# Kernel tuning notes

Measured on AMD Instinct MI355X. Metric: run time of the kernel, lower is better.

Reference implementation:

```python
import jax, jax.numpy as jnp
import numpy as np

N = 200_000      # num_nodes
D = 32           # embedding_dim
E = 6_400_000    # num edges (avg degree 32)
L = 3            # num_layers


def setup_inputs() -> dict:
    key = jax.random.key(0)
    k1, k2, k3, k4 = jax.random.split(key, 4)
    # xavier_uniform init: bound = sqrt(6 / (fan_in + fan_out))
    bound = float(np.sqrt(6.0 / (N + D)))
    embedding = jax.random.uniform(k1, (N, D), minval=-bound, maxval=bound, dtype=jnp.float32)
    row_idx = jax.random.randint(k2, (E,), 0, N, dtype=jnp.int32)
    col_idx = jax.random.randint(k3, (E,), 0, N, dtype=jnp.int32)
    # normalized adjacency values (roughly 1/degree scale, like sym-normalized LightGCN adj)
    vals = jax.random.uniform(k4, (E,), minval=0.0, maxval=2.0 / 32.0, dtype=jnp.float32)
    return {"embedding": embedding, "vals": vals, "row_idx": row_idx,
            "col_idx": col_idx, "num_layers": L}


def reference(embedding, vals, row_idx, col_idx, num_layers):
    # LightGCN propagation: e^{l+1} = A @ e^{l} (sparse COO SpMM via gather + scatter-add),
    # output = mean over layer outputs [e^0, e^1, ..., e^L].
    n = embedding.shape[0]
    e = embedding
    acc = embedding  # running sum of layer outputs (fused, avoids stacking)
    for _ in range(num_layers):
        msgs = vals[:, None] * e[col_idx]                      # [E, D] gather + scale
        e = jax.ops.segment_sum(msgs, row_idx, num_segments=n)  # [N, D] scatter-add
        acc = acc + e
    return acc / jnp.asarray(num_layers + 1, dtype=embedding.dtype)
```

## Files before the change

### kernel.cpp

```cpp
#include <hip/hip_runtime.h>
#include <hip/hip_bf16.h>

#define DIM 32
#define BSHIFT 8
#define BROWS 256
#define CAP 12288
#define CHUNK 8192
#define KMAX 1024


__global__ void lgcn_bhist(const int* __restrict__ row,
                           int* __restrict__ bcount, int E, int K) {
    __shared__ int h[KMAX];
    int t = threadIdx.x;
    for (int b = t; b < K; b += blockDim.x) h[b] = 0;
    __syncthreads();
    for (int i = blockIdx.x * blockDim.x + t; i < E; i += gridDim.x * blockDim.x)
        atomicAdd(&h[row[i] >> BSHIFT], 1);
    __syncthreads();
    for (int b = t; b < K; b += blockDim.x)
        if (h[b]) atomicAdd(&bcount[b], h[b]);
}

__global__ void lgcn_bscan(const int* __restrict__ bcount,
                           int* __restrict__ bbase, int* __restrict__ bcursor, int K) {
    __shared__ int s[1024];
    int t = threadIdx.x;
    int v = (t < K) ? bcount[t] : 0;
    s[t] = v;
    __syncthreads();
    for (int off = 1; off < 1024; off <<= 1) {
        int u = (t >= off) ? s[t - off] : 0;
        __syncthreads();
        s[t] += u;
        __syncthreads();
    }
    if (t < K) {
        int excl = s[t] - v;
        bbase[t] = excl;
        bcursor[t] = excl;
    }
    if (t == 0) bbase[K] = s[1023];
}

__launch_bounds__(1024)
__global__ void lgcn_bin(const int* __restrict__ row, const int* __restrict__ col,
                         const float* __restrict__ vals, int* __restrict__ bcursor,
                         int2* __restrict__ binned, int E, int K) {
    __shared__ int hh[KMAX];
    __shared__ int lb[KMAX + 1];
    __shared__ int cur[KMAX];
    __shared__ int2 sbuf[CHUNK];
    int t = threadIdx.x;
    int base = blockIdx.x * CHUNK;
    int cnt = E - base;
    if (cnt > CHUNK) cnt = CHUNK;

    for (int b = t; b < K; b += 1024) hh[b] = 0;
    __syncthreads();

    int  myb[CHUNK / 1024];
    int2 mycv[CHUNK / 1024];
    for (int k = 0; k < CHUNK / 1024; ++k) {
        int i = base + k * 1024 + t;
        if (i < base + cnt) {
            int r = row[i];
            myb[k] = r >> BSHIFT;
            mycv[k] = make_int2(col[i] | ((r & (BROWS - 1)) << 24),
                                __float_as_int(vals[i]));
            atomicAdd(&hh[myb[k]], 1);
        } else myb[k] = -1;
    }
    __syncthreads();

    int v = (t < K) ? hh[t] : 0;
    lb[t] = v;
    __syncthreads();
    for (int off = 1; off < 1024; off <<= 1) {
        int u = (t >= off) ? lb[t - off] : 0;
        __syncthreads();
        lb[t] += u;
        __syncthreads();
    }
    if (t == 0) lb[K] = cnt;
    int excl = lb[t] - v;
    __syncthreads();
    if (t < K) {
        lb[t] = excl;
        cur[t] = excl;
        int gbase = v ? atomicAdd(&bcursor[t], v) : 0;
        hh[t] = gbase - excl;
    }
    __syncthreads();

    for (int k = 0; k < CHUNK / 1024; ++k) {
        if (myb[k] >= 0) {
            int pos = atomicAdd(&cur[myb[k]], 1);
            sbuf[pos] = mycv[k];
        }
    }
    __syncthreads();

    for (int p = t; p < cnt; p += 1024) {
        int lo = 0, hi = K;
        while (hi - lo > 1) {
            int mid = (lo + hi) >> 1;
            if (lb[mid] <= p) lo = mid; else hi = mid;
        }
        binned[hh[lo] + p] = sbuf[p];
    }
}

__global__ void lgcn_bsort(const int* __restrict__ bbase,
                           int2* __restrict__ perm,
                           int* __restrict__ row_end, int N) {
    __shared__ int2 sorted[CAP];
    __shared__ int cnt[BROWS], scn[BROWS], cur[BROWS];
    int b = blockIdx.x, t = threadIdx.x;
    int sB = bbase[b], eB = bbase[b + 1];
    int nB = eB - sB;
    if (t < BROWS) cnt[t] = 0;
    __syncthreads();
    for (int i = sB + t; i < eB; i += 1024)
        atomicAdd(&cnt[(unsigned)perm[i].x >> 24], 1);
    __syncthreads();
    if (t < BROWS) scn[t] = cnt[t];
    __syncthreads();
    for (int off = 1; off < BROWS; off <<= 1) {
        int u = (t >= off && t < BROWS) ? scn[t - off] : 0;
        __syncthreads();
        if (t < BROWS) scn[t] += u;
        __syncthreads();
    }
    int g0 = b << BSHIFT;
    if (t < BROWS) {
        if (g0 + t < N) row_end[g0 + t] = sB + scn[t];
        cur[t] = scn[t] - cnt[t];
    }
    __syncthreads();
    for (int i = sB + t; i < eB; i += 1024) {
        int2 cv = perm[i];
        int r = (unsigned)cv.x >> 24;
        int p = atomicAdd(&cur[r], 1);
        if (p < CAP) sorted[p] = cv;
    }
    __syncthreads();
    for (int p = t; p < nB; p += 1024) {
        int pp = p < CAP ? p : CAP - 1;
        int2 cv = sorted[pp];
        perm[sB + p] = make_int2(cv.x & 0x00FFFFFF, cv.y);
    }
}

template <int MODE>
__global__ void lgcn_pull(const int* __restrict__ row_end,
                          const int2* __restrict__ perm,
                          const float* __restrict__ e_cur,
                          float* __restrict__ e_next,
                          const float* __restrict__ emb,
                          float* __restrict__ out, int N) {
    int g = blockIdx.x * (blockDim.x >> 5) + (threadIdx.x >> 5);
    if (g >= N) return;
    int d = threadIdx.x & 31;
    int beg = (g == 0) ? 0 : row_end[g - 1];
    int end = row_end[g];
    float acc = 0.f;
    int p = beg;
    for (; p + 3 < end; p += 4) {
        int2 cv0 = perm[p];
        int2 cv1 = perm[p + 1];
        int2 cv2 = perm[p + 2];
        int2 cv3 = perm[p + 3];
        acc = fmaf(__int_as_float(cv0.y), e_cur[(size_t)cv0.x * DIM + d], acc);
        acc = fmaf(__int_as_float(cv1.y), e_cur[(size_t)cv1.x * DIM + d], acc);
        acc = fmaf(__int_as_float(cv2.y), e_cur[(size_t)cv2.x * DIM + d], acc);
        acc = fmaf(__int_as_float(cv3.y), e_cur[(size_t)cv3.x * DIM + d], acc);
    }
    for (; p < end; ++p) {
        int2 cv = perm[p];
        acc = fmaf(__int_as_float(cv.y), e_cur[(size_t)cv.x * DIM + d], acc);
    }
    size_t o = (size_t)g * DIM + d;
    if (MODE == 0)      { e_next[o] = acc; out[o] = emb[o] + acc; }
    else if (MODE == 1) { e_next[o] = acc; out[o] += acc; }
    else                { out[o] = (out[o] + acc) * 0.25f; }
}


__global__ void lgcn_scatter(const float* __restrict__ e_cur,
                             float* __restrict__ e_next,
                             const float* __restrict__ vals,
                             const int* __restrict__ row_idx,
                             const int* __restrict__ col_idx, int E) {
    int g = blockIdx.x * (blockDim.x >> 5) + (threadIdx.x >> 5);
    if (g >= E) return;
    int d = threadIdx.x & 31;
    int c = col_idx[g];
    int r = row_idx[g];
    float v = vals[g];
    atomicAdd(&e_next[(size_t)r * DIM + d], v * e_cur[(size_t)c * DIM + d]);
}

__global__ void lgcn_add_init(const float* __restrict__ a, const float* __restrict__ b,
                              float* __restrict__ out, int n4) {
    int i = blockIdx.x * blockDim.x + threadIdx.x;
    if (i >= n4) return;
    float4 x = ((const float4*)a)[i]; float4 y = ((const float4*)b)[i];
    ((float4*)out)[i] = make_float4(x.x + y.x, x.y + y.y, x.z + y.z, x.w + y.w);
}
__global__ void lgcn_add(const float* __restrict__ b, float* __restrict__ out, int n4) {
    int i = blockIdx.x * blockDim.x + threadIdx.x;
    if (i >= n4) return;
    float4 x = ((float4*)out)[i]; float4 y = ((const float4*)b)[i];
    ((float4*)out)[i] = make_float4(x.x + y.x, x.y + y.y, x.z + y.z, x.w + y.w);
}
__global__ void lgcn_add_scale(const float* __restrict__ b, float* __restrict__ out,
                               int n4, float s) {
    int i = blockIdx.x * blockDim.x + threadIdx.x;
    if (i >= n4) return;
    float4 x = ((float4*)out)[i]; float4 y = ((const float4*)b)[i];
    ((float4*)out)[i] = make_float4((x.x + y.x) * s, (x.y + y.y) * s,
                                    (x.z + y.z) * s, (x.w + y.w) * s);
}

extern "C" void kernel_launch(void* const* d_in, const int* in_sizes, int n_in,
                              void* d_out, int out_size, void* d_ws, size_t ws_size,
                              hipStream_t stream) {
    const float* emb  = (const float*)d_in[0];
    const float* vals = (const float*)d_in[1];
    const int*   row  = (const int*)d_in[2];
    const int*   col  = (const int*)d_in[3];

    const int N = in_sizes[0] / DIM;
    const int E = in_sizes[1];
    float* out  = (float*)d_out;

    const int K = (N + BROWS - 1) >> BSHIFT;

    float* bufA    = (float*)d_ws;
    float* bufB    = bufA + (size_t)N * DIM;
    int*   row_end = (int*)(bufB + (size_t)N * DIM);
    int*   bcount  = row_end + N;
    int*   bbase   = bcount + K;
    int*   bcursor = bbase + (K + 1);
    size_t word_off = (size_t)((bcursor + K) - (int*)d_ws);
    word_off = (word_off + 1) & ~(size_t)1;
    int2*  perm    = (int2*)((int*)d_ws + word_off);
    const size_t needed = (word_off + (size_t)2 * E) * 4;

    const int n4 = N * DIM / 4;
    const int add_grid = (n4 + 255) / 256;
    const size_t layer_bytes = (size_t)N * DIM * sizeof(float);

    const double mean_bucket = (double)E / (double)N * BROWS;
    const bool csr_ok = (ws_size >= needed) && (K <= KMAX) &&
                        (mean_bucket * 1.45 < (double)CAP) &&
                        (N < (1 << 24));

    if (!csr_ok) {
        const int sct_grid = (E + 7) / 8;
        hipMemsetAsync(bufA, 0, layer_bytes, stream);
        lgcn_scatter<<<sct_grid, 256, 0, stream>>>(emb, bufA, vals, row, col, E);
        lgcn_add_init<<<add_grid, 256, 0, stream>>>(emb, bufA, out, n4);
        hipMemsetAsync(bufB, 0, layer_bytes, stream);
        lgcn_scatter<<<sct_grid, 256, 0, stream>>>(bufA, bufB, vals, row, col, E);
        lgcn_add<<<add_grid, 256, 0, stream>>>(bufB, out, n4);
        hipMemsetAsync(bufA, 0, layer_bytes, stream);
        lgcn_scatter<<<sct_grid, 256, 0, stream>>>(bufB, bufA, vals, row, col, E);
        lgcn_add_scale<<<add_grid, 256, 0, stream>>>(bufA, out, n4, 0.25f);
        return;
    }

    const int bin_grid = (E + CHUNK - 1) / CHUNK;
    hipMemsetAsync(bcount, 0, (size_t)K * sizeof(int), stream);
    lgcn_bhist<<<bin_grid, 256, 0, stream>>>(row, bcount, E, K);
    lgcn_bscan<<<1, 1024, 0, stream>>>(bcount, bbase, bcursor, K);
    lgcn_bin<<<bin_grid, 1024, 0, stream>>>(row, col, vals, bcursor, perm, E, K);
    lgcn_bsort<<<K, 1024, 0, stream>>>(bbase, perm, row_end, N);

    const int pull_grid = (N + 7) / 8;
    lgcn_pull<0><<<pull_grid, 256, 0, stream>>>(row_end, perm, emb, bufA, emb, out, N);
    lgcn_pull<1><<<pull_grid, 256, 0, stream>>>(row_end, perm, bufA, bufB, emb, out, N);
    lgcn_pull<2><<<pull_grid, 256, 0, stream>>>(row_end, perm, bufB, nullptr, emb, out, N);
}
```

Measured before the change: 539.1 us.

## Store layer embeddings as fp16 and split edges across half-warps in pull

Layer embeddings used for gathering are now stored as half2 (a conversion kernel creates an fp16 copy of the input embedding), which halves the bytes per random row gather. The pull kernel now has each half-warp process alternate edges with 16 lanes each loading a half2, then combines the two partial sums with a shuffle. Accumulation and the output stay fp32. The cost is an extra conversion pass and fp16 rounding of the intermediate layers, which may reduce accuracy.

```diff
diff --git a/kernel.cpp b/kernel.cpp
--- a/kernel.cpp
+++ b/kernel.cpp
@@ -1,5 +1,6 @@
 #include <hip/hip_runtime.h>
 #include <hip/hip_bf16.h>
+#include <hip/hip_fp16.h>
 
 #define DIM 32
 #define BSHIFT 8
@@ -152,38 +153,70 @@
     }
 }
 
+__global__ void lgcn_f2h(const float* __restrict__ src,
+                         __half2* __restrict__ dst, int n2) {
+    int i = blockIdx.x * blockDim.x + threadIdx.x;
+    if (i >= n2) return;
+    float2 v = ((const float2*)src)[i];
+    dst[i] = __float22half2_rn(v);
+}
+
 template <int MODE>
 __global__ void lgcn_pull(const int* __restrict__ row_end,
                           const int2* __restrict__ perm,
-                          const float* __restrict__ e_cur,
-                          float* __restrict__ e_next,
+                          const __half2* __restrict__ e_cur,
+                          __half2* __restrict__ e_next,
                           const float* __restrict__ emb,
                           float* __restrict__ out, int N) {
     int g = blockIdx.x * (blockDim.x >> 5) + (threadIdx.x >> 5);
     if (g >= N) return;
-    int d = threadIdx.x & 31;
+    int l = threadIdx.x & 31;
+    int sub = l >> 4;
+    int d2 = l & 15;
     int beg = (g == 0) ? 0 : row_end[g - 1];
     int end = row_end[g];
-    float acc = 0.f;
-    int p = beg;
-    for (; p + 3 < end; p += 4) {
-        int2 cv0 = perm[p];
-        int2 cv1 = perm[p + 1];
-        int2 cv2 = perm[p + 2];
-        int2 cv3 = perm[p + 3];
-        acc = fmaf(__int_as_float(cv0.y), e_cur[(size_t)cv0.x * DIM + d], acc);
-        acc = fmaf(__int_as_float(cv1.y), e_cur[(size_t)cv1.x * DIM + d], acc);
-        acc = fmaf(__int_as_float(cv2.y), e_cur[(size_t)cv2.x * DIM + d], acc);
-        acc = fmaf(__int_as_float(cv3.y), e_cur[(size_t)cv3.x * DIM + d], acc);
-    }
-    for (; p < end; ++p) {
+    float ax = 0.f, ay = 0.f;
+    int p = beg + sub;
+    for (; p + 6 < end; p += 8) {
+        int2 c0 = perm[p];
+        int2 c1 = perm[p + 2];
+        int2 c2 = perm[p + 4];
+        int2 c3 = perm[p + 6];
+        float2 x0 = __half22float2(e_cur[(size_t)c0.x * 16 + d2]);
+        float2 x1 = __half22float2(e_cur[(size_t)c1.x * 16 + d2]);
+        float2 x2 = __half22float2(e_cur[(size_t)c2.x * 16 + d2]);
+        float2 x3 = __half22float2(e_cur[(size_t)c3.x * 16 + d2]);
+        float v0 = __int_as_float(c0.y), v1 = __int_as_float(c1.y);
+        float v2 = __int_as_float(c2.y), v3 = __int_as_float(c3.y);
+        ax = fmaf(v0, x0.x, ax); ay = fmaf(v0, x0.y, ay);
+        ax = fmaf(v1, x1.x, ax); ay = fmaf(v1, x1.y, ay);
+        ax = fmaf(v2, x2.x, ax); ay = fmaf(v2, x2.y, ay);
+        ax = fmaf(v3, x3.x, ax); ay = fmaf(v3, x3.y, ay);
+    }
+    for (; p < end; p += 2) {
         int2 cv = perm[p];
-        acc = fmaf(__int_as_float(cv.y), e_cur[(size_t)cv.x * DIM + d], acc);
-    }
-    size_t o = (size_t)g * DIM + d;
-    if (MODE == 0)      { e_next[o] = acc; out[o] = emb[o] + acc; }
-    else if (MODE == 1) { e_next[o] = acc; out[o] += acc; }
-    else                { out[o] = (out[o] + acc) * 0.25f; }
+        float2 x = __half22float2(e_cur[(size_t)cv.x * 16 + d2]);
+        float v = __int_as_float(cv.y);
+        ax = fmaf(v, x.x, ax); ay = fmaf(v, x.y, ay);
+    }
+    ax += __shfl_xor(ax, 16);
+    ay += __shfl_xor(ay, 16);
+    if (sub == 0) {
+        size_t o2 = (size_t)g * 16 + d2;
+        if (MODE == 0) {
+            e_next[o2] = __float22half2_rn(make_float2(ax, ay));
+            float2 e0 = ((const float2*)emb)[o2];
+            ((float2*)out)[o2] = make_float2(e0.x + ax, e0.y + ay);
+        } else if (MODE == 1) {
+            e_next[o2] = __float22half2_rn(make_float2(ax, ay));
+            float2 c = ((float2*)out)[o2];
+            ((float2*)out)[o2] = make_float2(c.x + ax, c.y + ay);
+        } else {
+            float2 c = ((float2*)out)[o2];
+            ((float2*)out)[o2] = make_float2((c.x + ax) * 0.25f,
+                                             (c.y + ay) * 0.25f);
+        }
+    }
 }
 
 
@@ -237,9 +270,11 @@
 
     const int K = (N + BROWS - 1) >> BSHIFT;
 
-    float* bufA    = (float*)d_ws;
-    float* bufB    = bufA + (size_t)N * DIM;
-    int*   row_end = (int*)(bufB + (size_t)N * DIM);
+    const size_t hwords = (size_t)N * DIM / 2;
+    __half2* emb_h  = (__half2*)d_ws;
+    __half2* bufA_h = (__half2*)((int*)d_ws + hwords);
+    __half2* bufB_h = (__half2*)((int*)d_ws + 2 * hwords);
+    int*   row_end = (int*)d_ws + 3 * hwords;
     int*   bcount  = row_end + N;
     int*   bbase   = bcount + K;
     int*   bcursor = bbase + (K + 1);
@@ -249,15 +284,18 @@
     const size_t needed = (word_off + (size_t)2 * E) * 4;
 
     const int n4 = N * DIM / 4;
+    const int n2 = N * DIM / 2;
     const int add_grid = (n4 + 255) / 256;
     const size_t layer_bytes = (size_t)N * DIM * sizeof(float);
 
     const double mean_bucket = (double)E / (double)N * BROWS;
     const bool csr_ok = (ws_size >= needed) && (K <= KMAX) &&
                         (mean_bucket * 1.45 < (double)CAP) &&
-                        (N < (1 << 24));
+                        (N < (1 << 24)) && (DIM % 4 == 0);
 
     if (!csr_ok) {
+        float* bufA = (float*)d_ws;
+        float* bufB = bufA + (size_t)N * DIM;
         const int sct_grid = (E + 7) / 8;
         hipMemsetAsync(bufA, 0, layer_bytes, stream);
         lgcn_scatter<<<sct_grid, 256, 0, stream>>>(emb, bufA, vals, row, col, E);
@@ -273,13 +311,14 @@
 
     const int bin_grid = (E + CHUNK - 1) / CHUNK;
     hipMemsetAsync(bcount, 0, (size_t)K * sizeof(int), stream);
+    lgcn_f2h<<<(n2 + 255) / 256, 256, 0, stream>>>(emb, emb_h, n2);
     lgcn_bhist<<<bin_grid, 256, 0, stream>>>(row, bcount, E, K);
     lgcn_bscan<<<1, 1024, 0, stream>>>(bcount, bbase, bcursor, K);
     lgcn_bin<<<bin_grid, 1024, 0, stream>>>(row, col, vals, bcursor, perm, E, K);
     lgcn_bsort<<<K, 1024, 0, stream>>>(bbase, perm, row_end, N);
 
     const int pull_grid = (N + 7) / 8;
-    lgcn_pull<0><<<pull_grid, 256, 0, stream>>>(row_end, perm, emb, bufA, emb, out, N);
-    lgcn_pull<1><<<pull_grid, 256, 0, stream>>>(row_end, perm, bufA, bufB, emb, out, N);
-    lgcn_pull<2><<<pull_grid, 256, 0, stream>>>(row_end, perm, bufB, nullptr, emb, out, N);
-}
+    lgcn_pull<0><<<pull_grid, 256, 0, stream>>>(row_end, perm, emb_h, bufA_h, emb, out, N);
+    lgcn_pull<1><<<pull_grid, 256, 0, stream>>>(row_end, perm, bufA_h, bufB_h, emb, out, N);
+    lgcn_pull<2><<<pull_grid, 256, 0, stream>>>(row_end, perm, bufB_h, nullptr, emb, out, N);
+}
```

Measured after the change: 457.1 us. 1.18x faster.
